# Kernel optimization log

Hardware: AMD Instinct MI355X
Metric: run time of the kernel (lower is better)

## Reference

```python
import jax, jax.numpy as jnp
import numpy as np

EPS = 1e-12  # torch F.normalize eps

def _colnorm(w, g):
    # F.normalize(w, dim=0, p=2) * g  (column-wise L2 over dim 0)
    n = jnp.sqrt(jnp.sum(w * w, axis=0, keepdims=True))
    return (w / jnp.maximum(n, EPS)) * g

def setup_inputs() -> dict:
    key = jax.random.key(0)
    ks = jax.random.split(key, 16)
    B, T, V, E, H = 16, 512, 8192, 512, 1024
    inp = {
        'xs': jax.random.randint(ks[0], (B, T), 0, V),
        'ys': jax.random.randint(ks[1], (B, T), 0, V),
        'embed_w': jax.random.normal(ks[2], (V, E), jnp.float32) * 0.02,
        'wx': jax.random.normal(ks[3], (E, 4 * H), jnp.float32),
        'wh': jax.random.normal(ks[4], (H, 4 * H), jnp.float32),
        'wmx': jax.random.normal(ks[5], (E, H), jnp.float32),
        'wmh': jax.random.normal(ks[6], (H, H), jnp.float32),
        'b': jax.random.normal(ks[7], (4 * H,), jnp.float32) * 0.02,
        'gx': jax.random.normal(ks[8], (4 * H,), jnp.float32),
        'gh': jax.random.normal(ks[9], (4 * H,), jnp.float32),
        'gmx': jax.random.normal(ks[10], (H,), jnp.float32),
        'gmh': jax.random.normal(ks[11], (H,), jnp.float32),
        'pred_w': jax.random.normal(ks[12], (V, H), jnp.float32) * 0.02,
        'pred_b': jax.random.normal(ks[13], (V,), jnp.float32) * 0.02,
    }
    return inp

def reference(xs, ys, embed_w, wx, wh, wmx, wmh, b, gx, gh, gmx, gmh, pred_w, pred_b):
    B, T = xs.shape
    H = wmh.shape[0]
    V = pred_w.shape[0]
    # padding_idx=0 -> embedding row 0 is zero
    ew = embed_w.at[0].set(0.0)
    x = ew[xs]  # [B, T, E]
    # weight norm
    wx_n = _colnorm(wx, gx)
    wh_n = _colnorm(wh, gh)
    wmx_n = _colnorm(wmx, gmx)
    wmh_n = _colnorm(wmh, gmh)
    # precompute input-dependent projections (same math, batched over time)
    zx = jnp.einsum('bte,ef->btf', x, wx_n) + b     # [B, T, 4H]
    mx = jnp.einsum('bte,eh->bth', x, wmx_n)        # [B, T, H]

    def step(carry, inp):
        h, c = carry
        zx_t, mx_t = inp
        m = mx_t * (h @ wmh_n)                       # [B, H]
        z = zx_t + m @ wh_n                          # [B, 4H]
        i, f, o, u = jnp.split(z, 4, axis=1)
        i = jax.nn.sigmoid(i)
        f = jax.nn.sigmoid(f)
        o = jax.nn.sigmoid(o)
        u = jnp.tanh(u)
        c = f * c + i * u
        h = o * jnp.tanh(c)
        return (h, c), h

    h0 = jnp.zeros((B, H), x.dtype)
    c0 = jnp.zeros((B, H), x.dtype)
    _, hs = jax.lax.scan(step, (h0, c0), (zx.transpose(1, 0, 2), mx.transpose(1, 0, 2)))
    hs = hs.transpose(1, 0, 2)  # [B, T, H]
    logits = jnp.einsum('bth,vh->btv', hs, pred_w) + pred_b
    log_p = jax.nn.log_softmax(logits.reshape(B * T, V), axis=-1)
    nll = -jnp.take_along_axis(log_p, ys.reshape(B * T, 1), axis=1)
    return jnp.mean(nll)
```

## Files before the change

kernel.cpp:

```cpp
#include <hip/hip_runtime.h>
#include <hip/hip_bf16.h>
#include <stdint.h>

#define B_   16
#define T_   512
#define V_   8192
#define E_   512
#define H_   1024
#define BT_  (B_ * T_)
#define H4_  (4 * H_)

typedef __attribute__((ext_vector_type(8))) short   short8;
typedef __attribute__((ext_vector_type(8))) __bf16  bf16x8;
typedef __attribute__((ext_vector_type(4))) float   f32x4;
typedef __attribute__((ext_vector_type(4))) short   short4v;
typedef unsigned long long ull;

__device__ __forceinline__ float bf2f(short s) {
  union { unsigned u; float f; } x;
  x.u = ((unsigned)(unsigned short)s) << 16;
  return x.f;
}
__device__ __forceinline__ short f2bf(float f) {
  union { float f; unsigned u; } x; x.f = f;
  unsigned u = x.u;
  u = (u + 0x7fffu + ((u >> 16) & 1u)) >> 16;
  return (short)u;
}
__device__ __forceinline__ f32x4 mfma16(short8 a, short8 b, f32x4 c) {
  return __builtin_amdgcn_mfma_f32_16x16x32_bf16(
      __builtin_bit_cast(bf16x8, a), __builtin_bit_cast(bf16x8, b), c, 0, 0, 0);
}
__device__ __forceinline__ float sigm(float x) { return 1.f / (1.f + __expf(-x)); }
__device__ __forceinline__ float tanh_f(float x) { return 1.f - 2.f / (__expf(2.f * x) + 1.f); }

__device__ __forceinline__ short8 mk8(ull lo, ull hi) {
  union { ull u[2]; short8 s; } c;
  c.u[0] = lo; c.u[1] = hi;
  return c.s;
}

__global__ __launch_bounds__(256) void colscale(const float* __restrict__ W,
                                                const float* __restrict__ g,
                                                float* __restrict__ sc, int Kr, int N) {
  int j = blockIdx.x * 256 + threadIdx.x;
  if (j >= N) return;
  float ss = 0.f;
  for (int i = 0; i < Kr; ++i) { float v = W[(long)i * N + j]; ss = fmaf(v, v, ss); }
  sc[j] = g[j] / fmaxf(sqrtf(ss), 1e-12f);
}

__global__ __launch_bounds__(256) void transpose_cast(const float* __restrict__ W,
                                                      const float* __restrict__ sc,
                                                      short* __restrict__ WT, int Kr, int N) {
  __shared__ float tile[32][33];
  int nbi = Kr >> 5;
  int bi = blockIdx.x % nbi, bj = blockIdx.x / nbi;
  int i0 = bi << 5, j0 = bj << 5;
  int tx = threadIdx.x & 31, ty = threadIdx.x >> 5;
  for (int yy = ty; yy < 32; yy += 8)
    tile[yy][tx] = W[(long)(i0 + yy) * N + j0 + tx];
  __syncthreads();
  for (int yy = ty; yy < 32; yy += 8) {
    int j = j0 + yy;
    WT[(long)j * Kr + i0 + tx] = f2bf(tile[tx][yy] * sc[j]);
  }
}

__global__ __launch_bounds__(256) void castbf(const float* __restrict__ src,
                                              short* __restrict__ dst, long n) {
  long i = ((long)blockIdx.x * 256 + threadIdx.x) * 4;
  if (i + 3 < n) {
    float4 v = *(const float4*)(src + i);
    short4v o = { f2bf(v.x), f2bf(v.y), f2bf(v.z), f2bf(v.w) };
    *(short4v*)(dst + i) = o;
  }
}

__global__ __launch_bounds__(256) void embed_gather(const int* __restrict__ xs,
                                                    const float* __restrict__ ew,
                                                    short* __restrict__ x) {
  int r = blockIdx.x;
  int idx = xs[r];
  const float* src = ew + (long)idx * E_;
  for (int e = threadIdx.x; e < E_; e += 256) {
    float v = (idx == 0) ? 0.f : src[e];
    x[(long)r * E_ + e] = f2bf(v);
  }
}

__global__ __launch_bounds__(256) void gemm_bt(const short* __restrict__ A,
                                               const short* __restrict__ BT,
                                               const float* __restrict__ bias,
                                               short* __restrict__ C,
                                               int M, int N, int K) {
  int ntiles = N >> 7;
  int tM = (blockIdx.x / ntiles) << 7;
  int tN = (blockIdx.x % ntiles) << 7;
  int w = threadIdx.x >> 6, lane = threadIdx.x & 63;
  int mo = tM + ((w & 1) << 6), no = tN + ((w >> 1) << 6);
  int lr = lane & 15, lk8 = (lane >> 4) << 3, q = lane >> 4;
  f32x4 acc[4][4] = {};
  const short* Ap = A + (long)(mo + lr) * K + lk8;
  const short* Bp = BT + (long)(no + lr) * K + lk8;
  for (int k0 = 0; k0 < K; k0 += 32) {
    short8 af[4], bfr[4];
#pragma unroll
    for (int i = 0; i < 4; ++i) af[i] = *(const short8*)(Ap + (long)16 * i * K + k0);
#pragma unroll
    for (int j = 0; j < 4; ++j) bfr[j] = *(const short8*)(Bp + (long)16 * j * K + k0);
#pragma unroll
    for (int i = 0; i < 4; ++i)
#pragma unroll
      for (int j = 0; j < 4; ++j)
        acc[i][j] = mfma16(af[i], bfr[j], acc[i][j]);
  }
  float pbv[4];
#pragma unroll
  for (int j = 0; j < 4; ++j) pbv[j] = bias ? bias[no + 16 * j + lr] : 0.f;
#pragma unroll
  for (int i = 0; i < 4; ++i)
#pragma unroll
    for (int j = 0; j < 4; ++j)
#pragma unroll
      for (int r = 0; r < 4; ++r) {
        int row = mo + 16 * i + 4 * q + r;
        int col = no + 16 * j + lr;
        C[(long)row * N + col] = f2bf(acc[i][j][r] + pbv[j]);
      }
}

#define NWG_   64
#define NLOG_  192
#define NTILE_ 4096

__device__ __forceinline__ void logits_work(
    int tid,
    const short* __restrict__ hs, const short* __restrict__ pwb,
    const float* __restrict__ pb, const int* __restrict__ ys,
    float* __restrict__ sumexp, float* __restrict__ logit_y,
    unsigned* __restrict__ prog, unsigned* __restrict__ tile_ctr,
    int* s_sh) {
  const int w = tid >> 6, lane = tid & 63;
  const int lr = lane & 15, q = lane >> 4;
  const int lk8 = q << 3;
  int lastp = -1;
  for (;;) {
    __syncthreads();
    if (tid == 0) *s_sh = (int)atomicAdd(tile_ctr, 1u);
    __syncthreads();
    const int s = *s_sh;
    if (s >= NTILE_) break;
    const int p = s >> 10;
    if (p > lastp) {
      const unsigned target = (unsigned)((p + 1) << 7);
      while (__hip_atomic_load(prog + tid, __ATOMIC_RELAXED,
                               __HIP_MEMORY_SCOPE_AGENT) < target)
        __builtin_amdgcn_s_sleep(127);
      __syncthreads();
      lastp = p;
    }
    const int rem = s & 1023;
    const int bb = rem >> 6, vb = rem & 63;
    const int tM = ((bb << 2) + p) << 7;
    const int tN = vb << 7;
    const int mo = tM + ((w & 1) << 6), no = tN + ((w >> 1) << 6);
    f32x4 acc[4][4] = {};
    const short* Ap = hs + (long)(mo + lr) * H_ + lk8;
    const short* Bp = pwb + (long)(no + lr) * H_ + lk8;
    for (int k0 = 0; k0 < H_; k0 += 32) {
      short8 af[4], bfr[4];
#pragma unroll
      for (int i = 0; i < 4; ++i) af[i] = *(const short8*)(Ap + (long)16 * i * H_ + k0);
#pragma unroll
      for (int j = 0; j < 4; ++j) bfr[j] = *(const short8*)(Bp + (long)16 * j * H_ + k0);
#pragma unroll
      for (int i = 0; i < 4; ++i)
#pragma unroll
        for (int j = 0; j < 4; ++j)
          acc[i][j] = mfma16(af[i], bfr[j], acc[i][j]);
    }
    float pbv[4];
#pragma unroll
    for (int j = 0; j < 4; ++j) pbv[j] = pb[no + 16 * j + lr];
#pragma unroll
    for (int i = 0; i < 4; ++i) {
#pragma unroll
      for (int r = 0; r < 4; ++r) {
        int row = mo + 16 * i + 4 * q + r;
        int ysr = ys[row];
        float sum = 0.f;
#pragma unroll
        for (int j = 0; j < 4; ++j) {
          float v = acc[i][j][r] + pbv[j];
          sum += __expf(v);
          int col = no + 16 * j + lr;
          if (col == ysr) logit_y[row] = v;
        }
        sum += __shfl_xor(sum, 1); sum += __shfl_xor(sum, 2);
        sum += __shfl_xor(sum, 4); sum += __shfl_xor(sum, 8);
        if (lr == 0) atomicAdd(&sumexp[row], sum);
      }
    }
  }
}

__global__ __launch_bounds__(256, 1) void scan_logits(
    const short* __restrict__ zxb, const short* __restrict__ mxb,
    const short* __restrict__ wmhT, const short* __restrict__ whT,
    short* __restrict__ hs,
    ull* __restrict__ h_ex,
    ull* __restrict__ m_ex,
    unsigned* __restrict__ flags_m,
    unsigned* __restrict__ flags_h,
    unsigned* __restrict__ prog,
    unsigned* __restrict__ tile_ctr,
    const short* __restrict__ pwb,
    const float* __restrict__ pb,
    const int* __restrict__ ys,
    float* __restrict__ sumexp,
    float* __restrict__ logit_y) {
  const int blk = blockIdx.x;
  const int tid = threadIdx.x;
  const int w = tid >> 6, lane = tid & 63;
  const int lr = lane & 15, q = tid >> 4 & 0 ? 0 : (lane >> 4);

  __shared__ float red1[4][16][16];
  __shared__ float red2[4][4][16][16];
  __shared__ int   s_sh;

  if (blk < NWG_) {
    const int g = blk;
    const int colg = g << 4;
    const int b = tid >> 4, cl = tid & 15;

    short8 wmh_f[8];
#pragma unroll
    for (int kk = 0; kk < 8; ++kk) {
      const ull* p = (const ull*)(wmhT + (long)(colg + lr) * H_ + (w << 8) + (kk << 5) + (q << 3));
      ull lo = __hip_atomic_load(p, __ATOMIC_RELAXED, __HIP_MEMORY_SCOPE_WORKGROUP);
      ull hi = __hip_atomic_load(p + 1, __ATOMIC_RELAXED, __HIP_MEMORY_SCOPE_WORKGROUP);
      wmh_f[kk] = mk8(lo, hi);
    }
    short8 wh_f[4][8];
#pragma unroll
    for (int gt = 0; gt < 4; ++gt)
#pragma unroll
      for (int kk = 0; kk < 8; ++kk) {
        const ull* p = (const ull*)(whT + (long)(gt * H_ + colg + lr) * H_ + (w << 8) + (kk << 5) + (q << 3));
        ull lo = __hip_atomic_load(p, __ATOMIC_RELAXED, __HIP_MEMORY_SCOPE_WORKGROUP);
        ull hi = __hip_atomic_load(p + 1, __ATOMIC_RELAXED, __HIP_MEMORY_SCOPE_WORKGROUP);
        wh_f[gt][kk] = mk8(lo, hi);
      }

    float c = 0.f;
    const ull* hp = h_ex + lr * 256 + (w << 6) + (q << 1);
    const ull* mp = m_ex + lr * 256 + (w << 6) + (q << 1);
    const unsigned* fhp = flags_h + (((w << 4) + (lane >> 2)) * 4 + (lane & 3)) * 16;
    const unsigned* fmp = flags_m + ((w << 4) + lr) * 16;
    const int b2 = tid >> 2, ch = tid & 3;
    ull* m_st = m_ex + (b2 << 8) + (colg >> 2) + ch;
    unsigned* h_st = (unsigned*)h_ex + (((b << 10) + colg + cl) >> 1);

    for (int t = 0; t < T_; ++t) {
      long rrow = (long)(b * T_ + t);
      const short* zrow = zxb + rrow * H4_ + colg + cl;
      short z0p = zrow[0 * H_], z1p = zrow[1 * H_], z2p = zrow[2 * H_], z3p = zrow[3 * H_];
      ull mxq = 0;
      if (w == 0)
        mxq = *(const ull*)(mxb + (long)(b2 * T_ + t) * H_ + colg + (ch << 2));

      while (__hip_atomic_load(fhp, __ATOMIC_RELAXED, __HIP_MEMORY_SCOPE_AGENT)
             < (unsigned)t) {}

      ull lh[16];
#pragma unroll
      for (int kk = 0; kk < 8; ++kk) {
        lh[2 * kk]     = __hip_atomic_load(hp + (kk << 3),     __ATOMIC_RELAXED, __HIP_MEMORY_SCOPE_AGENT);
        lh[2 * kk + 1] = __hip_atomic_load(hp + (kk << 3) + 1, __ATOMIC_RELAXED, __HIP_MEMORY_SCOPE_AGENT);
      }
      f32x4 a1 = {};
#pragma unroll
      for (int kk = 0; kk < 8; ++kk)
        a1 = mfma16(mk8(lh[2 * kk], lh[2 * kk + 1]), wmh_f[kk], a1);
#pragma unroll
      for (int r = 0; r < 4; ++r) red1[w][q * 4 + r][lr] = a1[r];
      __syncthreads();

      if (w == 0) {
        union { short4v s; ull u; } pk;
        union { short4v s; ull u; } mxu; mxu.u = mxq;
#pragma unroll
        for (int u = 0; u < 4; ++u) {
          float s = red1[0][b2][(ch << 2) + u] + red1[1][b2][(ch << 2) + u] +
                    red1[2][b2][(ch << 2) + u] + red1[3][b2][(ch << 2) + u];
          pk.s[u] = f2bf(bf2f(mxu.s[u]) * s);
        }
        __hip_atomic_store(m_st, pk.u, __ATOMIC_RELAXED, __HIP_MEMORY_SCOPE_AGENT);
        __builtin_amdgcn_s_waitcnt(0);
        if (tid == 0)
          __hip_atomic_store(&flags_m[g << 4], (unsigned)(t + 1),
                             __ATOMIC_RELAXED, __HIP_MEMORY_SCOPE_AGENT);
      }

      while (__hip_atomic_load(fmp, __ATOMIC_RELAXED, __HIP_MEMORY_SCOPE_AGENT)
             < (unsigned)(t + 1)) {}

      ull lm[16];
#pragma unroll
      for (int kk = 0; kk < 8; ++kk) {
        lm[2 * kk]     = __hip_atomic_load(mp + (kk << 3),     __ATOMIC_RELAXED, __HIP_MEMORY_SCOPE_AGENT);
        lm[2 * kk + 1] = __hip_atomic_load(mp + (kk << 3) + 1, __ATOMIC_RELAXED, __HIP_MEMORY_SCOPE_AGENT);
      }
      f32x4 a2[4] = {};
#pragma unroll
      for (int kk = 0; kk < 8; ++kk) {
        short8 mf = mk8(lm[2 * kk], lm[2 * kk + 1]);
#pragma unroll
        for (int gt = 0; gt < 4; ++gt)
          a2[gt] = mfma16(mf, wh_f[gt][kk], a2[gt]);
      }
#pragma unroll
      for (int gt = 0; gt < 4; ++gt)
#pragma unroll
        for (int r = 0; r < 4; ++r)
          red2[w][gt][q * 4 + r][lr] = a2[gt][r];
      __syncthreads();

      {
        float zi = red2[0][0][b][cl] + red2[1][0][b][cl] + red2[2][0][b][cl] + red2[3][0][b][cl] + bf2f(z0p);
        float zf = red2[0][1][b][cl] + red2[1][1][b][cl] + red2[2][1][b][cl] + red2[3][1][b][cl] + bf2f(z1p);
        float zo = red2[0][2][b][cl] + red2[1][2][b][cl] + red2[2][2][b][cl] + red2[3][2][b][cl] + bf2f(z2p);
        float zu = red2[0][3][b][cl] + red2[1][3][b][cl] + red2[2][3][b][cl] + red2[3][3][b][cl] + bf2f(z3p);
        float ig = sigm(zi), fg = sigm(zf), og = sigm(zo), ug = tanh_f(zu);
        c = fg * c + ig * ug;
        float h = og * tanh_f(c);
        short hb = f2bf(h);
        unsigned hv = (unsigned)(unsigned short)hb;
        unsigned ov = (unsigned)__shfl_xor((int)hv, 1);
        unsigned packed = hv | (ov << 16);
        if ((lane & 1) == 0) {
          __hip_atomic_store(h_st, packed, __ATOMIC_RELAXED, __HIP_MEMORY_SCOPE_AGENT);
          __hip_atomic_store((unsigned*)hs + (((rrow << 10) + colg + cl) >> 1),
                             packed, __ATOMIC_RELAXED, __HIP_MEMORY_SCOPE_AGENT);
        }
        __builtin_amdgcn_s_waitcnt(0);
        if (lane == 0) {
          __hip_atomic_store(&flags_h[((g << 2) + w) << 4], (unsigned)(t + 1),
                             __ATOMIC_RELAXED, __HIP_MEMORY_SCOPE_AGENT);
          __hip_atomic_store(&prog[(g << 2) + w], (unsigned)(t + 1),
                             __ATOMIC_RELAXED, __HIP_MEMORY_SCOPE_AGENT);
        }
      }
    }
    logits_work(tid, hs, pwb, pb, ys, sumexp, logit_y, prog, tile_ctr, &s_sh);
  } else {
    logits_work(tid, hs, pwb, pb, ys, sumexp, logit_y, prog, tile_ctr, &s_sh);
  }
}

__global__ __launch_bounds__(256) void reduce_nll(const float* __restrict__ se,
                                                  const float* __restrict__ ly,
                                                  float* __restrict__ out) {
  __shared__ float buf[256];
  float s = 0.f;
  for (int r = threadIdx.x; r < BT_; r += 256)
    s += logf(se[r]) - ly[r];
  buf[threadIdx.x] = s;
  __syncthreads();
  for (int off = 128; off > 0; off >>= 1) {
    if (threadIdx.x < off) buf[threadIdx.x] += buf[threadIdx.x + off];
    __syncthreads();
  }
  if (threadIdx.x == 0) out[0] = buf[0] * (1.0f / BT_);
}

extern "C" void kernel_launch(void* const* d_in, const int* in_sizes, int n_in,
                              void* d_out, int out_size, void* d_ws, size_t ws_size,
                              hipStream_t stream) {
  const int*   xs     = (const int*)d_in[0];
  const int*   ys     = (const int*)d_in[1];
  const float* embw   = (const float*)d_in[2];
  const float* wx     = (const float*)d_in[3];
  const float* wh     = (const float*)d_in[4];
  const float* wmx    = (const float*)d_in[5];
  const float* wmh    = (const float*)d_in[6];
  const float* bias   = (const float*)d_in[7];
  const float* gx     = (const float*)d_in[8];
  const float* gh     = (const float*)d_in[9];
  const float* gmx    = (const float*)d_in[10];
  const float* gmh    = (const float*)d_in[11];
  const float* pred_w = (const float*)d_in[12];
  const float* pred_b = (const float*)d_in[13];
  float* out = (float*)d_out;

  char* base = (char*)d_ws;
  size_t off = 0;
  auto alloc = [&](size_t bytes) -> void* {
    void* p = base + off;
    off = (off + bytes + 255) & ~(size_t)255;
    return p;
  };
  short* xb     = (short*)alloc((size_t)BT_ * E_ * 2);
  short* zxb    = (short*)alloc((size_t)BT_ * H4_ * 2);
  short* mxb    = (short*)alloc((size_t)BT_ * H_ * 2);
  short* hs     = (short*)alloc((size_t)BT_ * H_ * 2);
  short* wxT    = (short*)alloc((size_t)H4_ * E_ * 2);
  short* whT    = (short*)alloc((size_t)H4_ * H_ * 2);
  short* wmxT   = (short*)alloc((size_t)H_ * E_ * 2);
  short* wmhT   = (short*)alloc((size_t)H_ * H_ * 2);
  short* pwb    = (short*)alloc((size_t)V_ * H_ * 2);
  float* scx    = (float*)alloc(H4_ * 4);
  float* sch    = (float*)alloc(H4_ * 4);
  float* scmx   = (float*)alloc(H_ * 4);
  float* scmh   = (float*)alloc(H_ * 4);
  float* l_y    = (float*)alloc(BT_ * 4);
  ull*   m_ex   = (ull*)alloc((size_t)B_ * H_ * 2);
  size_t z0 = off;
  float*    sumexp  = (float*)alloc(BT_ * 4);
  unsigned* flags_m = (unsigned*)alloc(NWG_ * 16 * 4);
  unsigned* flags_h = (unsigned*)alloc(NWG_ * 4 * 16 * 4);
  unsigned* prog    = (unsigned*)alloc(NWG_ * 4 * 4);
  unsigned* tile_ctr= (unsigned*)alloc(256);
  ull*      h_ex    = (ull*)alloc((size_t)B_ * H_ * 2);
  size_t zlen = off - z0;

  hipMemsetAsync(base + z0, 0, zlen, stream);

  colscale<<<H4_ / 256, 256, 0, stream>>>(wx, gx, scx, E_, H4_);
  colscale<<<H4_ / 256, 256, 0, stream>>>(wh, gh, sch, H_, H4_);
  colscale<<<H_ / 256, 256, 0, stream>>>(wmx, gmx, scmx, E_, H_);
  colscale<<<H_ / 256, 256, 0, stream>>>(wmh, gmh, scmh, H_, H_);
  transpose_cast<<<(E_ / 32) * (H4_ / 32), 256, 0, stream>>>(wx, scx, wxT, E_, H4_);
  transpose_cast<<<(H_ / 32) * (H4_ / 32), 256, 0, stream>>>(wh, sch, whT, H_, H4_);
  transpose_cast<<<(E_ / 32) * (H_ / 32), 256, 0, stream>>>(wmx, scmx, wmxT, E_, H_);
  transpose_cast<<<(H_ / 32) * (H_ / 32), 256, 0, stream>>>(wmh, scmh, wmhT, H_, H_);
  castbf<<<((long)V_ * H_) / 1024, 256, 0, stream>>>(pred_w, pwb, (long)V_ * H_);

  embed_gather<<<BT_, 256, 0, stream>>>(xs, embw, xb);
  gemm_bt<<<(BT_ / 128) * (H4_ / 128), 256, 0, stream>>>(xb, wxT, bias, zxb, BT_, H4_, E_);
  gemm_bt<<<(BT_ / 128) * (H_ / 128), 256, 0, stream>>>(xb, wmxT, nullptr, mxb, BT_, H_, E_);

  scan_logits<<<NWG_ + NLOG_, 256, 0, stream>>>(zxb, mxb, wmhT, whT, hs,
                                                h_ex, m_ex, flags_m, flags_h, prog,
                                                tile_ctr, pwb, pred_b, ys, sumexp, l_y);

  reduce_nll<<<1, 256, 0, stream>>>(sumexp, l_y, out);
}
```

Measured before the change: 5.899 ms.

## Replace dynamic logits tile queue with static staggered assignment and partial sums

The 192 logits workgroups now use a fixed mapping of vocab block and batch stripe instead of taking tiles from an atomic counter. Their readiness targets are staggered by vocab block so they start at different points of the scan and contend less with it. Per-row sum-of-exp goes into 128 partial slots rather than through float atomics, and a new row_nll kernel reduces those slots. The 64 scan workgroups no longer do logits work after the scan, so the end of the last phase may be less balanced, and a 4 MB partial buffer plus one extra kernel launch are added.

```diff
diff --git a/kernel.cpp b/kernel.cpp
--- a/kernel.cpp
+++ b/kernel.cpp
@@ -132,74 +132,64 @@
 
 #define NWG_   64
 #define NLOG_  192
-#define NTILE_ 4096
-
-__device__ __forceinline__ void logits_work(
-    int tid,
+
+__device__ __forceinline__ void logits_work_static(
+    int tid, int vb, int k3,
     const short* __restrict__ hs, const short* __restrict__ pwb,
     const float* __restrict__ pb, const int* __restrict__ ys,
-    float* __restrict__ sumexp, float* __restrict__ logit_y,
-    unsigned* __restrict__ prog, unsigned* __restrict__ tile_ctr,
-    int* s_sh) {
+    float* __restrict__ sumexp_p, float* __restrict__ logit_y,
+    unsigned* __restrict__ prog) {
   const int w = tid >> 6, lane = tid & 63;
   const int lr = lane & 15, q = lane >> 4;
   const int lk8 = q << 3;
-  int lastp = -1;
-  for (;;) {
+  const int tN = vb << 7;
+  const int no = tN + ((w >> 1) << 6);
+  float* sump_slot = sumexp_p + (((long)(vb << 1) | (w >> 1)) << 13);
+  float pbv[4];
+#pragma unroll
+  for (int j = 0; j < 4; ++j) pbv[j] = pb[no + 16 * j + lr];
+  for (int p = 0; p < 4; ++p) {
+    const unsigned target = (unsigned)(((p + 1) << 7) + ((p < 3) ? ((vb & 15) << 1) : 0));
+    while (__hip_atomic_load(prog + tid, __ATOMIC_RELAXED,
+                             __HIP_MEMORY_SCOPE_AGENT) < target)
+      __builtin_amdgcn_s_sleep(127);
     __syncthreads();
-    if (tid == 0) *s_sh = (int)atomicAdd(tile_ctr, 1u);
-    __syncthreads();
-    const int s = *s_sh;
-    if (s >= NTILE_) break;
-    const int p = s >> 10;
-    if (p > lastp) {
-      const unsigned target = (unsigned)((p + 1) << 7);
-      while (__hip_atomic_load(prog + tid, __ATOMIC_RELAXED,
-                               __HIP_MEMORY_SCOPE_AGENT) < target)
-        __builtin_amdgcn_s_sleep(127);
-      __syncthreads();
-      lastp = p;
-    }
-    const int rem = s & 1023;
-    const int bb = rem >> 6, vb = rem & 63;
-    const int tM = ((bb << 2) + p) << 7;
-    const int tN = vb << 7;
-    const int mo = tM + ((w & 1) << 6), no = tN + ((w >> 1) << 6);
-    f32x4 acc[4][4] = {};
-    const short* Ap = hs + (long)(mo + lr) * H_ + lk8;
-    const short* Bp = pwb + (long)(no + lr) * H_ + lk8;
-    for (int k0 = 0; k0 < H_; k0 += 32) {
-      short8 af[4], bfr[4];
-#pragma unroll
-      for (int i = 0; i < 4; ++i) af[i] = *(const short8*)(Ap + (long)16 * i * H_ + k0);
-#pragma unroll
-      for (int j = 0; j < 4; ++j) bfr[j] = *(const short8*)(Bp + (long)16 * j * H_ + k0);
-#pragma unroll
-      for (int i = 0; i < 4; ++i)
-#pragma unroll
-        for (int j = 0; j < 4; ++j)
-          acc[i][j] = mfma16(af[i], bfr[j], acc[i][j]);
-    }
-    float pbv[4];
-#pragma unroll
-    for (int j = 0; j < 4; ++j) pbv[j] = pb[no + 16 * j + lr];
-#pragma unroll
-    for (int i = 0; i < 4; ++i) {
-#pragma unroll
-      for (int r = 0; r < 4; ++r) {
-        int row = mo + 16 * i + 4 * q + r;
-        int ysr = ys[row];
-        float sum = 0.f;
-#pragma unroll
-        for (int j = 0; j < 4; ++j) {
-          float v = acc[i][j][r] + pbv[j];
-          sum += __expf(v);
-          int col = no + 16 * j + lr;
-          if (col == ysr) logit_y[row] = v;
+    for (int bb = k3; bb < 16; bb += 3) {
+      const int tM = ((bb << 2) + p) << 7;
+      const int mo = tM + ((w & 1) << 6);
+      f32x4 acc[4][4] = {};
+      const short* Ap = hs + (long)(mo + lr) * H_ + lk8;
+      const short* Bp = pwb + (long)(no + lr) * H_ + lk8;
+      for (int k0 = 0; k0 < H_; k0 += 32) {
+        short8 af[4], bfr[4];
+#pragma unroll
+        for (int i = 0; i < 4; ++i) af[i] = *(const short8*)(Ap + (long)16 * i * H_ + k0);
+#pragma unroll
+        for (int j = 0; j < 4; ++j) bfr[j] = *(const short8*)(Bp + (long)16 * j * H_ + k0);
+#pragma unroll
+        for (int i = 0; i < 4; ++i)
+#pragma unroll
+          for (int j = 0; j < 4; ++j)
+            acc[i][j] = mfma16(af[i], bfr[j], acc[i][j]);
+      }
+#pragma unroll
+      for (int i = 0; i < 4; ++i) {
+#pragma unroll
+        for (int r = 0; r < 4; ++r) {
+          int row = mo + 16 * i + 4 * q + r;
+          int ysr = ys[row];
+          float sum = 0.f;
+#pragma unroll
+          for (int j = 0; j < 4; ++j) {
+            float v = acc[i][j][r] + pbv[j];
+            sum += __expf(v);
+            int col = no + 16 * j + lr;
+            if (col == ysr) logit_y[row] = v;
+          }
+          sum += __shfl_xor(sum, 1); sum += __shfl_xor(sum, 2);
+          sum += __shfl_xor(sum, 4); sum += __shfl_xor(sum, 8);
+          if (lr == 0) sump_slot[row] = sum;
         }
-        sum += __shfl_xor(sum, 1); sum += __shfl_xor(sum, 2);
-        sum += __shfl_xor(sum, 4); sum += __shfl_xor(sum, 8);
-        if (lr == 0) atomicAdd(&sumexp[row], sum);
       }
     }
   }
@@ -214,20 +204,18 @@
     unsigned* __restrict__ flags_m,
     unsigned* __restrict__ flags_h,
     unsigned* __restrict__ prog,
-    unsigned* __restrict__ tile_ctr,
     const short* __restrict__ pwb,
     const float* __restrict__ pb,
     const int* __restrict__ ys,
-    float* __restrict__ sumexp,
+    float* __restrict__ sumexp_p,
     float* __restrict__ logit_y) {
   const int blk = blockIdx.x;
   const int tid = threadIdx.x;
   const int w = tid >> 6, lane = tid & 63;
-  const int lr = lane & 15, q = tid >> 4 & 0 ? 0 : (lane >> 4);
+  const int lr = lane & 15, q = lane >> 4;
 
   __shared__ float red1[4][16][16];
   __shared__ float red2[4][4][16][16];
-  __shared__ int   s_sh;
 
   if (blk < NWG_) {
     const int g = blk;
@@ -353,19 +341,29 @@
         }
       }
     }
-    logits_work(tid, hs, pwb, pb, ys, sumexp, logit_y, prog, tile_ctr, &s_sh);
   } else {
-    logits_work(tid, hs, pwb, pb, ys, sumexp, logit_y, prog, tile_ctr, &s_sh);
-  }
-}
-
-__global__ __launch_bounds__(256) void reduce_nll(const float* __restrict__ se,
-                                                  const float* __restrict__ ly,
+    const int wid = blk - NWG_;
+    const int vb  = ((wid & 7) << 3) | ((wid >> 3) & 7);
+    const int k3  = wid >> 6;
+    logits_work_static(tid, vb, k3, hs, pwb, pb, ys, sumexp_p, logit_y, prog);
+  }
+}
+
+__global__ __launch_bounds__(256) void row_nll(const float* __restrict__ sumexp_p,
+                                               const float* __restrict__ ly,
+                                               float* __restrict__ nll) {
+  int r = blockIdx.x * 256 + threadIdx.x;
+  float s = 0.f;
+  for (int vb2 = 0; vb2 < 128; ++vb2) s += sumexp_p[((long)vb2 << 13) + r];
+  nll[r] = logf(s) - ly[r];
+}
+
+__global__ __launch_bounds__(256) void reduce_nll(const float* __restrict__ nll,
                                                   float* __restrict__ out) {
   __shared__ float buf[256];
   float s = 0.f;
   for (int r = threadIdx.x; r < BT_; r += 256)
-    s += logf(se[r]) - ly[r];
+    s += nll[r];
   buf[threadIdx.x] = s;
   __syncthreads();
   for (int off = 128; off > 0; off >>= 1) {
@@ -415,13 +413,13 @@
   float* scmx   = (float*)alloc(H_ * 4);
   float* scmh   = (float*)alloc(H_ * 4);
   float* l_y    = (float*)alloc(BT_ * 4);
+  float* sump   = (float*)alloc((size_t)128 * BT_ * 4);
+  float* nll    = (float*)alloc(BT_ * 4);
   ull*   m_ex   = (ull*)alloc((size_t)B_ * H_ * 2);
   size_t z0 = off;
-  float*    sumexp  = (float*)alloc(BT_ * 4);
   unsigned* flags_m = (unsigned*)alloc(NWG_ * 16 * 4);
   unsigned* flags_h = (unsigned*)alloc(NWG_ * 4 * 16 * 4);
   unsigned* prog    = (unsigned*)alloc(NWG_ * 4 * 4);
-  unsigned* tile_ctr= (unsigned*)alloc(256);
   ull*      h_ex    = (ull*)alloc((size_t)B_ * H_ * 2);
   size_t zlen = off - z0;
 
@@ -443,7 +441,8 @@
 
   scan_logits<<<NWG_ + NLOG_, 256, 0, stream>>>(zxb, mxb, wmhT, whT, hs,
                                                 h_ex, m_ex, flags_m, flags_h, prog,
-                                                tile_ctr, pwb, pred_b, ys, sumexp, l_y);
-
-  reduce_nll<<<1, 256, 0, stream>>>(sumexp, l_y, out);
-}
+                                                pwb, pred_b, ys, sump, l_y);
+
+  row_nll<<<BT_ / 256, 256, 0, stream>>>(sump, l_y, nll);
+  reduce_nll<<<1, 256, 0, stream>>>(nll, out);
+}
```

Result: slower. 6.022 ms (+2.1%).
